# Performance work log

Measured on AMD Instinct MI355X. Metric: run time of the kernel, lower is better.

Reference implementation:

```python
import jax, jax.numpy as jnp
import numpy as np

# dims: batch, history P, horizon Q, hidden D, nodes N, cells C=H*W, Z channels
B_, P_, Q_, D_, N_, C_, H_, W_, CZ = 16, 12, 12, 64, 2000, 1024, 32, 32, 2
K_DIFF = 3  # max diffusion step of DCGRUCell -> K+1 Chebyshev terms


def _mlp2(x, w1, b1, w2, b2):
    return jax.nn.relu(x @ w1 + b1) @ w2 + b2


def _st_embedding(SE, TE, sw1, sb1, sw2, sb2, tw1, tb1, tw2, tb2):
    # GMAN-style spatio-temporal embedding: SE (M,D), TE (B,P,2) ints
    se = _mlp2(SE, sw1, sb1, sw2, sb2)                                  # (M, D)
    te = jnp.concatenate([jax.nn.one_hot(TE[..., 0], 7, dtype=SE.dtype),
                          jax.nn.one_hot(TE[..., 1], 288, dtype=SE.dtype)], axis=-1)
    te = _mlp2(te, tw1, tb1, tw2, tb2)                                  # (B, P, D)
    return se[None, None] + te[:, :, None, :]                           # (B, P, M, D)


def _scaled_laplacian(adj):
    # DCRNN 'laplacian' filter: L_tilde = 2 L / lambda_max - I, lambda_max ~= 2
    A = jnp.maximum(adj, adj.T)
    d = A.sum(axis=1)
    dinv = jnp.where(d > 0, jax.lax.rsqrt(d), 0.0)
    eye = jnp.eye(A.shape[0], dtype=A.dtype)
    L = eye - (dinv[:, None] * A) * dinv[None, :]
    return L - eye


def _gconv(x, L, K):
    # Chebyshev diffusion features: x (B,N,F) -> (B,N,F*(K+1))
    xs = [x, jnp.einsum('nm,bmf->bnf', L, x)]
    for _ in range(2, K + 1):
        xs.append(2.0 * jnp.einsum('nm,bmf->bnf', L, xs[-1]) - xs[-2])
    b, n, f = x.shape
    return jnp.stack(xs, axis=-1).reshape(b, n, f * (K + 1))


def _hard_sigmoid(x):
    return jnp.clip(0.2 * x + 0.5, 0.0, 1.0)


def _conv2d(x, w):
    return jax.lax.conv_general_dilated(x, w, (1, 1), 'SAME',
        dimension_numbers=('NHWC', 'HWIO', 'NHWC'))


def _forward(X, Z, TE, adj_gg, adj_gr, gumbel_noise, se_x, se_z, movement_logits,
             stex_se_w1, stex_se_b1, stex_se_w2, stex_se_b2,
             stex_te_w1, stex_te_b1, stex_te_w2, stex_te_b2,
             stez_se_w1, stez_se_b1, stez_se_w2, stez_se_b2,
             stez_te_w1, stez_te_b1, stez_te_w2, stez_te_b2,
             fcs_z_w1, fcs_z_b1, fcs_z_w2, fcs_z_b2,
             fcs_x_in_w1, fcs_x_in_b1, fcs_x_in_w2, fcs_x_in_b2,
             mov_fc_w, mov_fc_b,
             fcs_x_out_w1, fcs_x_out_b1, fcs_x_out_w2, fcs_x_out_b2,
             convlstm_wx, convlstm_wh,
             dcgru_gate_w, dcgru_gate_b, dcgru_cand_w, dcgru_cand_b):
    B = X.shape[0]
    TEp = TE.astype(jnp.int32)[:, :P_, :]
    # --- cell branch ---
    STEZ = _st_embedding(se_z, TEp, stez_se_w1, stez_se_b1, stez_se_w2, stez_se_b2,
                         stez_te_w1, stez_te_b1, stez_te_w2, stez_te_b2)
    Zf = _mlp2(Z, fcs_z_w1, fcs_z_b1, fcs_z_w2, fcs_z_b2) + STEZ          # (B,P,C,D)
    Zg = Zf.reshape(B, P_, H_, W_, D_)
    def clstm_step(carry, x):
        h, c = carry
        gates = _conv2d(x, convlstm_wx) + _conv2d(h, convlstm_wh)         # (B,H,W,4D)
        i, f, g, o = jnp.split(gates, 4, axis=-1)
        c = _hard_sigmoid(f) * c + _hard_sigmoid(i) * jnp.tanh(g)
        h = _hard_sigmoid(o) * jnp.tanh(c)
        return (h, c), h
    hc0 = (jnp.zeros((B, H_, W_, D_), X.dtype), jnp.zeros((B, H_, W_, D_), X.dtype))
    _, hs = jax.lax.scan(clstm_step, hc0, jnp.swapaxes(Zg, 0, 1))
    Zc = jnp.swapaxes(hs, 0, 1).reshape(B, P_, C_, D_)
    # gumbel-softmax routing over cells (soft, tau=1)
    g = -jnp.log(-jnp.log(gumbel_noise + 1e-20) + 1e-20)
    mZ = jax.nn.softmax(movement_logits + g, axis=-1)                     # (C,C)
    Zc = jnp.einsum('cd,bpdk->bpck', mZ, Zc)
    Zc = jax.nn.relu(Zc @ mov_fc_w + mov_fc_b)
    ZX = jnp.einsum('nc,bpck->bpnk', adj_gr, Zc)                          # (B,P,N,D)
    # --- node branch ---
    STEX = _st_embedding(se_x, TEp, stex_se_w1, stex_se_b1, stex_se_w2, stex_se_b2,
                         stex_te_w1, stex_te_b1, stex_te_w2, stex_te_b2)
    Xf = _mlp2(X[..., None], fcs_x_in_w1, fcs_x_in_b1, fcs_x_in_w2, fcs_x_in_b2) + STEX + ZX
    L = _scaled_laplacian(adj_gg)
    def dcgru_step(h, x):
        xh = jnp.concatenate([x, h], axis=-1)                             # (B,N,2D)
        ru = jax.nn.sigmoid(_gconv(xh, L, K_DIFF) @ dcgru_gate_w + dcgru_gate_b)
        r, u = jnp.split(ru, 2, axis=-1)
        cnd = jnp.tanh(_gconv(jnp.concatenate([x, r * h], axis=-1), L, K_DIFF)
                       @ dcgru_cand_w + dcgru_cand_b)
        return u * h + (1.0 - u) * cnd, None
    h_last, _ = jax.lax.scan(dcgru_step, jnp.zeros((B, N_, D_), X.dtype),
                             jnp.swapaxes(Xf, 0, 1))                      # (B,N,D)
    Y = _mlp2(h_last, fcs_x_out_w1, fcs_x_out_b1, fcs_x_out_w2, fcs_x_out_b2)  # (B,N,Q)
    return jnp.transpose(Y, (0, 2, 1))                                    # (B,Q,N)


def setup_inputs() -> dict:
    key = jax.random.key(0)
    ks = iter(jax.random.split(key, 64))
    def rn(shape, s=0.05):
        return jax.random.normal(next(ks), shape, dtype=jnp.float32) * s
    def ru(shape):
        return jax.random.uniform(next(ks), shape, dtype=jnp.float32)
    z = lambda *s: jnp.zeros(s, jnp.float32)
    NM = K_DIFF + 1
    inp = {
        'X': rn((B_, P_, N_), 1.0),
        'Z': rn((B_, P_, C_, CZ), 1.0),
        'TE': jax.random.randint(next(ks), (B_, P_ + Q_, 2), 0, 7, dtype=jnp.int32),
        'adj_gg': ru((N_, N_)),
        'adj_gr': ru((N_, C_)) * 0.01,
        'gumbel_noise': jnp.clip(ru((C_, C_)), 1e-6, 1.0 - 1e-6),
        'se_x': rn((N_, D_)), 'se_z': rn((C_, D_)),
        'movement_logits': rn((C_, C_)),
        'stex_se_w1': rn((D_, D_)), 'stex_se_b1': z(D_), 'stex_se_w2': rn((D_, D_)), 'stex_se_b2': z(D_),
        'stex_te_w1': rn((295, D_)), 'stex_te_b1': z(D_), 'stex_te_w2': rn((D_, D_)), 'stex_te_b2': z(D_),
        'stez_se_w1': rn((D_, D_)), 'stez_se_b1': z(D_), 'stez_se_w2': rn((D_, D_)), 'stez_se_b2': z(D_),
        'stez_te_w1': rn((295, D_)), 'stez_te_b1': z(D_), 'stez_te_w2': rn((D_, D_)), 'stez_te_b2': z(D_),
        'fcs_z_w1': rn((CZ, D_)), 'fcs_z_b1': z(D_), 'fcs_z_w2': rn((D_, D_)), 'fcs_z_b2': z(D_),
        'fcs_x_in_w1': rn((1, D_)), 'fcs_x_in_b1': z(D_), 'fcs_x_in_w2': rn((D_, D_)), 'fcs_x_in_b2': z(D_),
        'mov_fc_w': rn((D_, D_)), 'mov_fc_b': z(D_),
        'fcs_x_out_w1': rn((D_, D_)), 'fcs_x_out_b1': z(D_), 'fcs_x_out_w2': rn((D_, Q_)), 'fcs_x_out_b2': z(Q_),
        'convlstm_wx': rn((3, 3, D_, 4 * D_)), 'convlstm_wh': rn((3, 3, D_, 4 * D_)),
        'dcgru_gate_w': rn((2 * D_ * NM, 2 * D_)), 'dcgru_gate_b': z(2 * D_),
        'dcgru_cand_w': rn((2 * D_ * NM, D_)), 'dcgru_cand_b': z(D_),
    }
    return inp


def reference(X, Z, TE, adj_gg, adj_gr, gumbel_noise, se_x, se_z, movement_logits,
              stex_se_w1, stex_se_b1, stex_se_w2, stex_se_b2,
              stex_te_w1, stex_te_b1, stex_te_w2, stex_te_b2,
              stez_se_w1, stez_se_b1, stez_se_w2, stez_se_b2,
              stez_te_w1, stez_te_b1, stez_te_w2, stez_te_b2,
              fcs_z_w1, fcs_z_b1, fcs_z_w2, fcs_z_b2,
              fcs_x_in_w1, fcs_x_in_b1, fcs_x_in_w2, fcs_x_in_b2,
              mov_fc_w, mov_fc_b,
              fcs_x_out_w1, fcs_x_out_b1, fcs_x_out_w2, fcs_x_out_b2,
              convlstm_wx, convlstm_wh,
              dcgru_gate_w, dcgru_gate_b, dcgru_cand_w, dcgru_cand_b):
    return _forward(X, Z, TE, adj_gg, adj_gr, gumbel_noise, se_x, se_z, movement_logits,
                    stex_se_w1, stex_se_b1, stex_se_w2, stex_se_b2,
                    stex_te_w1, stex_te_b1, stex_te_w2, stex_te_b2,
                    stez_se_w1, stez_se_b1, stez_se_w2, stez_se_b2,
                    stez_te_w1, stez_te_b1, stez_te_w2, stez_te_b2,
                    fcs_z_w1, fcs_z_b1, fcs_z_w2, fcs_z_b2,
                    fcs_x_in_w1, fcs_x_in_b1, fcs_x_in_w2, fcs_x_in_b2,
                    mov_fc_w, mov_fc_b,
                    fcs_x_out_w1, fcs_x_out_b1, fcs_x_out_w2, fcs_x_out_b2,
                    convlstm_wx, convlstm_wh,
                    dcgru_gate_w, dcgru_gate_b, dcgru_cand_w, dcgru_cand_b)
```

## Files before the change

kernel.cpp:

```cpp
#include <hip/hip_runtime.h>
#include <hip/hip_bf16.h>
#include <math.h>

typedef _Float16 fp16;
typedef _Float16 f16x8 __attribute__((ext_vector_type(8)));
typedef float f32x4 __attribute__((ext_vector_type(4)));

#define BB 16
#define PP 12
#define QQ 12
#define NN 2000
#define CC 1024
#define GP 34
#define GP2 1156

static __device__ __forceinline__ float ldf(float v) { return v; }
static __device__ __forceinline__ float ldf(fp16 v) { return (float)v; }
static __device__ __forceinline__ void stf(float* p, float v) { *p = v; }
static __device__ __forceinline__ void stf(fp16* p, float v) { *p = (fp16)v; }

static __device__ __forceinline__ void gload_lds16(const fp16* g, fp16* l) {
  __builtin_amdgcn_global_load_lds(
      (const __attribute__((address_space(1))) void*)g,
      (__attribute__((address_space(3))) void*)l, 16, 0, 0);
}

__global__ void k_f2h(fp16* __restrict__ dst, const float* __restrict__ src, long long n) {
  long long i = (long long)blockIdx.x * 256 + threadIdx.x;
  if (i < n) dst[i] = (fp16)src[i];
}

__global__ void k_wcatT(fp16* __restrict__ dst, const float* __restrict__ w39,
                        const float* __restrict__ w40) {
  int i = blockIdx.x * 256 + threadIdx.x;
  if (i >= 1152 * 256) return;
  int n = i & 255, kk = i >> 8;
  float v = (kk < 576) ? w39[kk * 256 + n] : w40[(kk - 576) * 256 + n];
  dst[(long long)n * 1152 + kk] = (fp16)v;
}

__global__ void k_gru_repackT(fp16* __restrict__ dst, const float* __restrict__ src, int O) {
  int i = blockIdx.x * 256 + threadIdx.x;
  if (i >= O * 512) return;
  int d = i >> 9;
  int kc = i & 511;
  int t = kc >> 7;
  int c = kc & 127;
  dst[i] = (fp16)src[(c * 4 + t) * O + d];
}

__global__ void k_w2T(fp16* __restrict__ dst, const float* __restrict__ src) {
  int i = blockIdx.x * 256 + threadIdx.x;
  if (i >= 4096) return;
  int d = i >> 6, k = i & 63;
  dst[i] = (fp16)src[k * 64 + d];
}

__global__ void k_dinv(const float* __restrict__ adj, float* __restrict__ dinv) {
  int row = blockIdx.x;
  float s = 0.f;
  for (int j = threadIdx.x; j < NN; j += 256)
    s += fmaxf(adj[(long long)row * NN + j], adj[(long long)j * NN + row]);
  __shared__ float red[256];
  red[threadIdx.x] = s;
  __syncthreads();
  for (int st = 128; st > 0; st >>= 1) {
    if (threadIdx.x < st) red[threadIdx.x] += red[threadIdx.x + st];
    __syncthreads();
  }
  if (threadIdx.x == 0) {
    float d = red[0];
    dinv[row] = d > 0.f ? 1.0f / sqrtf(d) : 0.f;
  }
}

__global__ void k_L(const float* __restrict__ adj, const float* __restrict__ dinv,
                    fp16* __restrict__ Lh) {
  long long i = (long long)blockIdx.x * 256 + threadIdx.x;
  if (i >= (long long)NN * NN) return;
  int r = (int)(i / NN), c = (int)(i % NN);
  float a = fmaxf(adj[(long long)r * NN + c], adj[(long long)c * NN + r]);
  Lh[(long long)r * 2048 + c] = (fp16)(-dinv[r] * a * dinv[c]);
}

__global__ void k_subdiag(fp16* __restrict__ M2) {
  int i = blockIdx.x * 256 + threadIdx.x;
  if (i >= NN) return;
  M2[(long long)i * 2048 + i] = (fp16)((float)M2[(long long)i * 2048 + i] - 1.0f);
}

__global__ void k_gumbel_softmax(const float* __restrict__ ml, const float* __restrict__ gn,
                                 fp16* __restrict__ mZ) {
  int row = blockIdx.x;
  __shared__ float buf[CC];
  __shared__ float red[256];
  int t = threadIdx.x;
  float mx = -1e30f;
  for (int j = t; j < CC; j += 256) {
    float u = gn[(long long)row * CC + j];
    float g = -logf(-logf(u + 1e-20f) + 1e-20f);
    float v = ml[(long long)row * CC + j] + g;
    buf[j] = v;
    mx = fmaxf(mx, v);
  }
  red[t] = mx;
  __syncthreads();
  for (int st = 128; st > 0; st >>= 1) {
    if (t < st) red[t] = fmaxf(red[t], red[t + st]);
    __syncthreads();
  }
  mx = red[0];
  __syncthreads();
  float s = 0.f;
  for (int j = t; j < CC; j += 256) {
    float e = expf(buf[j] - mx);
    buf[j] = e;
    s += e;
  }
  red[t] = s;
  __syncthreads();
  for (int st = 128; st > 0; st >>= 1) {
    if (t < st) red[t] += red[t + st];
    __syncthreads();
  }
  float inv = 1.0f / red[0];
  for (int j = t; j < CC; j += 256) mZ[(long long)row * CC + j] = (fp16)(buf[j] * inv);
}

__global__ void k_te(const int* __restrict__ TE, const float* __restrict__ w1,
                     const float* __restrict__ b1, float* __restrict__ tmp) {
  int i = blockIdx.x * 256 + threadIdx.x;
  if (i >= BB * PP * 64) return;
  int j = i & 63;
  int bp = i >> 6;
  int b = bp / PP, p = bp % PP;
  int te0 = TE[(b * (PP + QQ) + p) * 2 + 0];
  int te1 = TE[(b * (PP + QQ) + p) * 2 + 1];
  float v = w1[te0 * 64 + j] + w1[(7 + te1) * 64 + j] + b1[j];
  tmp[i] = fmaxf(v, 0.f);
}

__global__ void k_addb(float* __restrict__ dst, const float* __restrict__ b, int n) {
  int i = blockIdx.x * 256 + threadIdx.x;
  if (i < n) dst[i] += b[i & 63];
}

__global__ void k_zf1(const float* __restrict__ Z, const float* __restrict__ w1,
                      const float* __restrict__ b1, fp16* __restrict__ tmp) {
  long long i = (long long)blockIdx.x * 256 + threadIdx.x;
  if (i >= (long long)BB * PP * CC * 64) return;
  int j = (int)(i & 63);
  long long row = i >> 6;
  float v = Z[row * 2 + 0] * w1[j] + Z[row * 2 + 1] * w1[64 + j] + b1[j];
  tmp[i] = (fp16)fmaxf(v, 0.f);
}

__global__ void k_add_stez(fp16* __restrict__ dst, const fp16* __restrict__ src,
                           const float* __restrict__ seZ, const float* __restrict__ teZ) {
  long long i = (long long)blockIdx.x * 256 + threadIdx.x;
  if (i >= (long long)BB * PP * CC * 64) return;
  int j = (int)(i & 63);
  long long row = i >> 6;
  int c = (int)(row & 1023);
  int bp = (int)(row >> 10);
  int pc = ((c >> 5) + 1) * GP + (c & 31) + 1;
  dst[((long long)bp * GP2 + pc) * 64 + j] =
      (fp16)((float)src[i] + seZ[c * 64 + j] + teZ[bp * 64 + j]);
}

template <typename TA, typename TB, typename TC>
__global__ __launch_bounds__(256) void gemm_t(
    const TA* __restrict__ A, int lda, long long sA,
    const TB* __restrict__ Bm, int ldb, long long sB,
    TC* Cm, int ldc, long long sC,
    const TC* S, long long sS,
    const float* __restrict__ bias,
    int M, int Ncols, int K, float alpha, float beta, int act) {
  int bz = blockIdx.z;
  A += (long long)bz * sA;
  Bm += (long long)bz * sB;
  Cm += (long long)bz * sC;
  if (S) S += (long long)bz * sS;
  const int row0 = blockIdx.x * 64, col0 = blockIdx.y * 64;
  __shared__ float As[16][68];
  __shared__ float Bs[16][68];
  int tid = threadIdx.x, tx = tid & 15, ty = tid >> 4;
  float acc[4][4] = {};
  for (int k0 = 0; k0 < K; k0 += 16) {
#pragma unroll
    for (int j = 0; j < 4; ++j) {
      int e = tid + 256 * j;
      int m = e >> 4, kk = e & 15;
      int gm = row0 + m;
      As[kk][m] = (gm < M) ? ldf(A[(long long)gm * lda + k0 + kk]) : 0.f;
    }
#pragma unroll
    for (int j = 0; j < 4; ++j) {
      int e = tid + 256 * j;
      int kk = e >> 6, n = e & 63;
      int gn = col0 + n;
      Bs[kk][n] = (gn < Ncols) ? ldf(Bm[(long long)(k0 + kk) * ldb + gn]) : 0.f;
    }
    __syncthreads();
#pragma unroll
    for (int kk = 0; kk < 16; ++kk) {
      float a[4], bb[4];
#pragma unroll
      for (int i = 0; i < 4; ++i) a[i] = As[kk][ty * 4 + i];
#pragma unroll
      for (int j = 0; j < 4; ++j) bb[j] = Bs[kk][tx * 4 + j];
#pragma unroll
      for (int i = 0; i < 4; ++i)
#pragma unroll
        for (int j = 0; j < 4; ++j) acc[i][j] = fmaf(a[i], bb[j], acc[i][j]);
    }
    __syncthreads();
  }
#pragma unroll
  for (int i = 0; i < 4; ++i) {
    int r = row0 + ty * 4 + i;
    if (r >= M) continue;
#pragma unroll
    for (int j = 0; j < 4; ++j) {
      int cn = col0 + tx * 4 + j;
      if (cn >= Ncols) continue;
      float v = alpha * acc[i][j];
      if (bias) v += bias[cn];
      if (S) v += beta * ldf(S[(long long)r * ldc + cn]);
      if (act == 1) v = fmaxf(v, 0.f);
      else if (act == 2) v = 1.f / (1.f + expf(-v));
      else if (act == 3) v = tanhf(v);
      stf(&Cm[(long long)r * ldc + cn], v);
    }
  }
}

template <int MT, int MODE>
__global__ __launch_bounds__(256) void mfma5(
    const fp16* __restrict__ A, int lda,
    const fp16* __restrict__ U0base, long long uZ, int bHi,
    const fp16* __restrict__ xB, long long xZ,
    const fp16* __restrict__ Tn, long long TnSlab,
    const fp16* __restrict__ Tn2, long long Tn2Slab,
    fp16* __restrict__ C, int ldc, long long cBatch,
    const float* __restrict__ bias,
    fp16* __restrict__ rhOut, const fp16* __restrict__ hIn,
    const fp16* __restrict__ uIn, long long uStride,
    int M, int Ncols, int K) {
  __shared__ fp16 As[MT][40];
  __shared__ fp16 Bs[64][40];
  const int z = blockIdx.z;
  const int gm0 = blockIdx.x * MT, n0 = blockIdx.y * 64;
  const fp16* U0z = U0base + (long long)z * uZ;
  const fp16* xBz = xB + (long long)z * xZ;
  C += (long long)z * cBatch;
  if (rhOut) rhOut += (long long)z * uZ;
  if (hIn) hIn += (long long)z * uZ;
  if (uIn) uIn += (long long)z * uStride;
  const int tid = threadIdx.x;
  const int lane = tid & 63, wv = tid >> 6;
  const int wr = wv >> 1, wc = wv & 1;
  const int quad = lane >> 4, ln = lane & 15;
  constexpr int WM = MT / 32;
  f32x4 acc[WM][2];
#pragma unroll
  for (int i = 0; i < WM; ++i)
#pragma unroll
    for (int j = 0; j < 2; ++j) acc[i][j] = (f32x4){0.f, 0.f, 0.f, 0.f};

  for (int k0 = 0; k0 < K; k0 += 32) {
#pragma unroll
    for (int i = 0; i < MT / 64; ++i) {
      int c = tid + 256 * i;
      int row = c >> 2, seg = c & 3;
      *(f16x8*)&As[row][seg * 8] =
          *(const f16x8*)(A + (long long)(gm0 + row) * lda + k0 + seg * 8);
    }
    {
      int slab = k0 >> 7;
      if (slab == 0) {
        int kin = k0 + (tid & 31);
        int ngrp = tid >> 5;
        int n = n0 + ngrp * 8;
        const fp16* src = (kin < 64) ? (xBz + (long long)kin * 2048 + n)
                                     : (U0z + (long long)(kin + bHi) * 2048 + n);
        f16x8 v = *(const f16x8*)src;
#pragma unroll
        for (int j = 0; j < 8; ++j) Bs[ngrp * 8 + j][tid & 31] = v[j];
      } else {
        int n = tid >> 2, seg = tid & 3;
        int kin0 = (k0 & 127) + seg * 8;
        long long node = n0 + n;
        const fp16* src;
        if (MODE == 1 || kin0 < 64)
          src = Tn + (long long)(slab - 1) * TnSlab + node * 2048 + z * 128 + kin0;
        else
          src = Tn2 + (long long)(slab - 1) * Tn2Slab + node * 1024 + z * 64 + (kin0 - 64);
        *(f16x8*)&Bs[n][seg * 8] = *(const f16x8*)src;
      }
    }
    __syncthreads();
    f16x8 af[WM], bf[2];
#pragma unroll
    for (int wm = 0; wm < WM; ++wm)
      af[wm] = *(const f16x8*)&As[wr * (MT / 2) + wm * 16 + ln][quad * 8];
#pragma unroll
    for (int wn = 0; wn < 2; ++wn)
      bf[wn] = *(const f16x8*)&Bs[wc * 32 + wn * 16 + ln][quad * 8];
#pragma unroll
    for (int wm = 0; wm < WM; ++wm)
#pragma unroll
      for (int wn = 0; wn < 2; ++wn)
        acc[wm][wn] =
            __builtin_amdgcn_mfma_f32_16x16x32_f16(af[wm], bf[wn], acc[wm][wn], 0, 0, 0);
    __syncthreads();
  }
#pragma unroll
  for (int wm = 0; wm < WM; ++wm) {
#pragma unroll
    for (int wn = 0; wn < 2; ++wn) {
#pragma unroll
      for (int r = 0; r < 4; ++r) {
        int gm = gm0 + wr * (MT / 2) + wm * 16 + quad * 4 + r;
        int gn = n0 + wc * 32 + wn * 16 + ln;
        if (gm < M && gn < Ncols) {
          float v = acc[wm][wn][r];
          v += bias[gm];
          if (MODE == 1) {
            v = 1.f / (1.f + expf(-v));
            C[(long long)gm * ldc + gn] = (fp16)v;
            if (gm < 64) {
              float h = (float)hIn[(long long)gm * 2048 + gn];
              rhOut[(long long)gm * 2048 + gn] = (fp16)(v * h);
            }
          } else {
            v = tanhf(v);
            float u = (float)uIn[(long long)(64 + gm) * NN + gn];
            long long ci = (long long)gm * ldc + gn;
            float h = (float)C[ci];
            C[ci] = (fp16)(u * h + (1.f - u) * v);
          }
        }
      }
    }
  }
}

template <int MT, int NT>
__global__ __launch_bounds__(256) void mfma3(
    const fp16* __restrict__ A, int lda, long long zA, int aMsh, long long aMslab,
    const fp16* __restrict__ B, int ldb, long long zB,
    fp16* __restrict__ C, int ldc, long long zC, int cMsh, long long cMslab, int cNsh,
    long long cNslab,
    const fp16* __restrict__ S, long long zS, float beta,
    const float* __restrict__ rowBias, long long zRB,
    const float* __restrict__ s2T, int s2ld,
    int M, int Ncols, int K, float alpha, int act) {
  __shared__ fp16 As[MT][40];
  __shared__ fp16 Bs[NT][40];
  const int z = blockIdx.z;
  const int gm0 = blockIdx.x * MT, n0 = blockIdx.y * NT;
  A += (long long)z * zA;
  B += (long long)z * zB;
  C += (long long)z * zC;
  if (S) S += (long long)z * zS;
  const int tid = threadIdx.x;
  const int lane = tid & 63, wv = tid >> 6;
  const int wr = wv >> 1, wc = wv & 1;
  const int quad = lane >> 4, ln = lane & 15;
  const unsigned aMmask = (1u << aMsh) - 1u;
  const unsigned cMmask = (1u << cMsh) - 1u;
  const unsigned cNmask = (1u << cNsh) - 1u;
  constexpr int WM = MT / 32, WN = NT / 32;
  f32x4 acc[WM][WN];
#pragma unroll
  for (int i = 0; i < WM; ++i)
#pragma unroll
    for (int j = 0; j < WN; ++j) acc[i][j] = (f32x4){0.f, 0.f, 0.f, 0.f};

  for (int k0 = 0; k0 < K; k0 += 32) {
#pragma unroll
    for (int i = 0; i < MT / 64; ++i) {
      int c = tid + 256 * i;
      int row = c >> 2, seg = c & 3;
      int gm = gm0 + row;
      int kk0 = k0 + seg * 8;
      const fp16* src = A + ((long long)((unsigned)gm >> aMsh)) * aMslab +
                        (long long)(gm & aMmask) * lda + kk0;
      if (gm < M && kk0 + 8 <= K) {
        *(f16x8*)&As[row][seg * 8] = *(const f16x8*)src;
      } else {
#pragma unroll
        for (int j = 0; j < 8; ++j)
          As[row][seg * 8 + j] = (gm < M && kk0 + j < K) ? src[j] : (fp16)0.f;
      }
    }
#pragma unroll
    for (int i = 0; i < NT / 64; ++i) {
      int c = tid + 256 * i;
      int n = c >> 2, seg = c & 3;
      int gn = n0 + n;
      int kk0 = k0 + seg * 8;
      const fp16* src = B + (long long)gn * ldb + kk0;
      if (gn < Ncols && kk0 + 8 <= K) {
        *(f16x8*)&Bs[n][seg * 8] = *(const f16x8*)src;
      } else {
#pragma unroll
        for (int j = 0; j < 8; ++j)
          Bs[n][seg * 8 + j] = (gn < Ncols && kk0 + j < K) ? src[j] : (fp16)0.f;
      }
    }
    __syncthreads();
    f16x8 af[WM], bf[WN];
#pragma unroll
    for (int wm = 0; wm < WM; ++wm)
      af[wm] = *(const f16x8*)&As[wr * (MT / 2) + wm * 16 + ln][quad * 8];
#pragma unroll
    for (int wn = 0; wn < WN; ++wn)
      bf[wn] = *(const f16x8*)&Bs[wc * (NT / 2) + wn * 16 + ln][quad * 8];
#pragma unroll
    for (int wm = 0; wm < WM; ++wm)
#pragma unroll
      for (int wn = 0; wn < WN; ++wn)
        acc[wm][wn] =
            __builtin_amdgcn_mfma_f32_16x16x32_f16(af[wm], bf[wn], acc[wm][wn], 0, 0, 0);
    __syncthreads();
  }
#pragma unroll
  for (int wm = 0; wm < WM; ++wm) {
#pragma unroll
    for (int wn = 0; wn < WN; ++wn) {
#pragma unroll
      for (int r = 0; r < 4; ++r) {
        int gm = gm0 + wr * (MT / 2) + wm * 16 + quad * 4 + r;
        int gn = n0 + wc * (NT / 2) + wn * 16 + ln;
        if (gm < M && gn < Ncols) {
          float v = alpha * acc[wm][wn][r];
          if (rowBias) v += rowBias[(long long)z * zRB + gm];
          if (s2T) v += s2T[(long long)gn * s2ld + gm];
          long long ci = ((long long)((unsigned)gm >> cMsh)) * cMslab +
                         (long long)(gm & cMmask) * ldc +
                         ((long long)((unsigned)gn >> cNsh)) * cNslab + (gn & cNmask);
          if (S) v += beta * (float)S[ci];
          if (act == 1) v = fmaxf(v, 0.f);
          else if (act == 2) v = 1.f / (1.f + expf(-v));
          else if (act == 3) v = tanhf(v);
          C[ci] = (fp16)v;
        }
      }
    }
  }
}

template <int MT, int NT>
__global__ __launch_bounds__(256) void mfma4(
    const fp16* __restrict__ base0, const fp16* __restrict__ base1, int rsh, int ssh,
    long long z0, long long z1, int lda,
    const fp16* __restrict__ B, int ldb, long long zB,
    fp16* __restrict__ C, int ldc, long long zC, int cMsh, long long cMslab, int cNsh,
    long long cNslab,
    const fp16* __restrict__ S, float alpha, float beta, int K) {
  __shared__ fp16 As[2][MT * 32];
  __shared__ fp16 Bs[2][NT * 32];
  const int tid = threadIdx.x;
  const int z = blockIdx.z;
  const int gm0 = blockIdx.x * MT, n0 = blockIdx.y * NT;
  B += (long long)z * zB;
  C += (long long)z * zC;
  if (S) S += (long long)z * zC;
  const unsigned cMmask = (1u << cMsh) - 1u;
  const unsigned cNmask = (1u << cNsh) - 1u;
  const int lane = tid & 63, wv = tid >> 6;
  const int wr = wv >> 1, wc = wv & 1;
  const int quad = lane >> 4, ln = lane & 15;
  constexpr int WM = MT / 32, WN = NT / 32;

  const fp16* aSrc[MT / 64];
  const fp16* bSrc[NT / 64];
#pragma unroll
  for (int i = 0; i < MT / 64; ++i) {
    int c = i * 256 + tid;
    int row = c >> 2;
    int lseg = (c & 3) ^ (row & 3);
    int gm = gm0 + row;
    unsigned b = (unsigned)gm >> rsh;
    unsigned wi = (unsigned)gm & ((1u << rsh) - 1u);
    unsigned sel = wi >> ssh;
    unsigned r = wi & ((1u << ssh) - 1u);
    const fp16* ab = sel ? (base1 + (long long)b * z1) : (base0 + (long long)b * z0);
    aSrc[i] = ab + (long long)r * lda + lseg * 8;
  }
#pragma unroll
  for (int i = 0; i < NT / 64; ++i) {
    int c = i * 256 + tid;
    int row = c >> 2;
    int lseg = (c & 3) ^ (row & 3);
    bSrc[i] = B + (long long)(n0 + row) * ldb + lseg * 8;
  }

  f32x4 acc[WM][WN];
#pragma unroll
  for (int i = 0; i < WM; ++i)
#pragma unroll
    for (int j = 0; j < WN; ++j) acc[i][j] = (f32x4){0.f, 0.f, 0.f, 0.f};

  const int sw = (quad ^ (ln & 3)) << 3;

#pragma unroll
  for (int i = 0; i < MT / 64; ++i) gload_lds16(aSrc[i], &As[0][(i * 256 + tid) * 8]);
#pragma unroll
  for (int i = 0; i < NT / 64; ++i) gload_lds16(bSrc[i], &Bs[0][(i * 256 + tid) * 8]);

  const int nk = K >> 5;
  for (int t = 0; t < nk; ++t) {
    const int buf = t & 1;
    __syncthreads();
    if (t + 1 < nk) {
      const int k1 = (t + 1) * 32;
#pragma unroll
      for (int i = 0; i < MT / 64; ++i)
        gload_lds16(aSrc[i] + k1, &As[buf ^ 1][(i * 256 + tid) * 8]);
#pragma unroll
      for (int i = 0; i < NT / 64; ++i)
        gload_lds16(bSrc[i] + k1, &Bs[buf ^ 1][(i * 256 + tid) * 8]);
    }
    f16x8 af[WM], bf[WN];
#pragma unroll
    for (int wm = 0; wm < WM; ++wm) {
      int row = wr * (MT / 2) + wm * 16 + ln;
      af[wm] = *(const f16x8*)&As[buf][row * 32 + sw];
    }
#pragma unroll
    for (int wn = 0; wn < WN; ++wn) {
      int row = wc * (NT / 2) + wn * 16 + ln;
      bf[wn] = *(const f16x8*)&Bs[buf][row * 32 + sw];
    }
#pragma unroll
    for (int wm = 0; wm < WM; ++wm)
#pragma unroll
      for (int wn = 0; wn < WN; ++wn)
        acc[wm][wn] =
            __builtin_amdgcn_mfma_f32_16x16x32_f16(af[wm], bf[wn], acc[wm][wn], 0, 0, 0);
  }
#pragma unroll
  for (int wm = 0; wm < WM; ++wm)
#pragma unroll
    for (int wn = 0; wn < WN; ++wn)
#pragma unroll
      for (int r = 0; r < 4; ++r) {
        int gm = gm0 + wr * (MT / 2) + wm * 16 + quad * 4 + r;
        int gn = n0 + wc * (NT / 2) + wn * 16 + ln;
        long long ci = ((long long)((unsigned)gm >> cMsh)) * cMslab +
                       (long long)(gm & cMmask) * ldc +
                       ((long long)((unsigned)gn >> cNsh)) * cNslab + (gn & cNmask);
        float v = alpha * acc[wm][wn][r];
        if (S) v += beta * (float)S[ci];
        C[ci] = (fp16)v;
      }
}

template <int MT, int NT>
__global__ __launch_bounds__(256) void mfma6(
    const fp16* __restrict__ A, int lda,
    const fp16* __restrict__ b0, const fp16* __restrict__ b1, int rsh, int ssh,
    long long z0, long long z1, int ldb,
    fp16* __restrict__ C, int ldc, int cMsh, long long cMslab,
    int K) {
  __shared__ fp16 As[2][MT * 32];
  __shared__ fp16 Bs[2][NT * 32];
  const int tid = threadIdx.x;
  const int gm0 = blockIdx.x * MT, n0 = blockIdx.y * NT;
  const unsigned cMmask = (1u << cMsh) - 1u;
  const int lane = tid & 63, wv = tid >> 6;
  const int wr = wv >> 1, wc = wv & 1;
  const int quad = lane >> 4, ln = lane & 15;
  constexpr int WM = MT / 32, WN = NT / 32;

  const fp16* aSrc[MT / 64];
  const fp16* bSrc[NT / 64];
#pragma unroll
  for (int i = 0; i < MT / 64; ++i) {
    int c = i * 256 + tid;
    int row = c >> 2;
    int lseg = (c & 3) ^ (row & 3);
    aSrc[i] = A + (long long)(gm0 + row) * lda + lseg * 8;
  }
#pragma unroll
  for (int i = 0; i < NT / 64; ++i) {
    int c = i * 256 + tid;
    int row = c >> 2;
    int lseg = (c & 3) ^ (row & 3);
    int gn = n0 + row;
    unsigned b = (unsigned)gn >> rsh;
    unsigned wi = (unsigned)gn & ((1u << rsh) - 1u);
    unsigned sel = wi >> ssh;
    unsigned r = wi & ((1u << ssh) - 1u);
    const fp16* bb = sel ? (b1 + (long long)b * z1) : (b0 + (long long)b * z0);
    bSrc[i] = bb + (long long)r * ldb + lseg * 8;
  }

  f32x4 acc[WM][WN];
#pragma unroll
  for (int i = 0; i < WM; ++i)
#pragma unroll
    for (int j = 0; j < WN; ++j) acc[i][j] = (f32x4){0.f, 0.f, 0.f, 0.f};

  const int sw = (quad ^ (ln & 3)) << 3;

#pragma unroll
  for (int i = 0; i < MT / 64; ++i) gload_lds16(aSrc[i], &As[0][(i * 256 + tid) * 8]);
#pragma unroll
  for (int i = 0; i < NT / 64; ++i) gload_lds16(bSrc[i], &Bs[0][(i * 256 + tid) * 8]);

  const int nk = K >> 5;
  for (int t = 0; t < nk; ++t) {
    const int buf = t & 1;
    __syncthreads();
    if (t + 1 < nk) {
      const int k1 = (t + 1) * 32;
#pragma unroll
      for (int i = 0; i < MT / 64; ++i)
        gload_lds16(aSrc[i] + k1, &As[buf ^ 1][(i * 256 + tid) * 8]);
#pragma unroll
      for (int i = 0; i < NT / 64; ++i)
        gload_lds16(bSrc[i] + k1, &Bs[buf ^ 1][(i * 256 + tid) * 8]);
    }
    f16x8 af[WM], bf[WN];
#pragma unroll
    for (int wm = 0; wm < WM; ++wm) {
      int row = wr * (MT / 2) + wm * 16 + ln;
      af[wm] = *(const f16x8*)&As[buf][row * 32 + sw];
    }
#pragma unroll
    for (int wn = 0; wn < WN; ++wn) {
      int row = wc * (NT / 2) + wn * 16 + ln;
      bf[wn] = *(const f16x8*)&Bs[buf][row * 32 + sw];
    }
#pragma unroll
    for (int wm = 0; wm < WM; ++wm)
#pragma unroll
      for (int wn = 0; wn < WN; ++wn)
        acc[wm][wn] =
            __builtin_amdgcn_mfma_f32_16x16x32_f16(af[wm], bf[wn], acc[wm][wn], 0, 0, 0);
  }
#pragma unroll
  for (int wm = 0; wm < WM; ++wm)
#pragma unroll
    for (int wn = 0; wn < WN; ++wn)
#pragma unroll
      for (int r = 0; r < 4; ++r) {
        int gm = gm0 + wr * (MT / 2) + wm * 16 + quad * 4 + r;
        int gn = n0 + wc * (NT / 2) + wn * 16 + ln;
        long long ci = ((long long)((unsigned)gm >> cMsh)) * cMslab +
                       (long long)(gm & cMmask) * ldc + gn;
        C[ci] = (fp16)acc[wm][wn][r];
      }
}

__global__ __launch_bounds__(256) void k_zxtfin(
    const fp16* __restrict__ w2T, const fp16* __restrict__ Tmat,
    fp16* __restrict__ ZXt, const float* __restrict__ teXb, const float* __restrict__ seX) {
  __shared__ fp16 As[64][72];
  __shared__ fp16 Bs[128][72];
  const int z = blockIdx.z;
  const int n0 = blockIdx.y * 128;
  const fp16* Tz = Tmat + (long long)z * 2048 * 64;
  fp16* Cz = ZXt + (long long)z * 64 * 2048;
  const float* tb = teXb + z * 64;
  const int tid = threadIdx.x;
  const int lane = tid & 63, wv = tid >> 6;
  const int wr = wv >> 1, wc = wv & 1;
  const int quad = lane >> 4, ln = lane & 15;
#pragma unroll
  for (int i = 0; i < 2; ++i) {
    int c = tid + 256 * i;
    int row = c >> 3, seg = c & 7;
    *(f16x8*)&As[row][seg * 8] = *(const f16x8*)(w2T + row * 64 + seg * 8);
  }
#pragma unroll
  for (int i = 0; i < 4; ++i) {
    int c = tid + 256 * i;
    int row = c >> 3, seg = c & 7;
    *(f16x8*)&Bs[row][seg * 8] =
        *(const f16x8*)(Tz + (long long)(n0 + row) * 64 + seg * 8);
  }
  __syncthreads();
  f32x4 acc[2][4];
#pragma unroll
  for (int i = 0; i < 2; ++i)
#pragma unroll
    for (int j = 0; j < 4; ++j) acc[i][j] = (f32x4){0.f, 0.f, 0.f, 0.f};
#pragma unroll
  for (int kt = 0; kt < 2; ++kt) {
    f16x8 af[2], bf[4];
#pragma unroll
    for (int wm = 0; wm < 2; ++wm)
      af[wm] = *(const f16x8*)&As[wr * 32 + wm * 16 + ln][kt * 32 + quad * 8];
#pragma unroll
    for (int wn = 0; wn < 4; ++wn)
      bf[wn] = *(const f16x8*)&Bs[wc * 64 + wn * 16 + ln][kt * 32 + quad * 8];
#pragma unroll
    for (int wm = 0; wm < 2; ++wm)
#pragma unroll
      for (int wn = 0; wn < 4; ++wn)
        acc[wm][wn] =
            __builtin_amdgcn_mfma_f32_16x16x32_f16(af[wm], bf[wn], acc[wm][wn], 0, 0, 0);
  }
#pragma unroll
  for (int wm = 0; wm < 2; ++wm)
#pragma unroll
    for (int wn = 0; wn < 4; ++wn)
#pragma unroll
      for (int r = 0; r < 4; ++r) {
        int gm = wr * 32 + wm * 16 + quad * 4 + r;
        int gn = n0 + wc * 64 + wn * 16 + ln;
        long long ci = (long long)gm * 2048 + gn;
        float v = 0.f;
        if (gn < NN)
          v = acc[wm][wn][r] + (float)Cz[ci] + tb[gm] + seX[(long long)gn * 64 + gm];
        Cz[ci] = (fp16)v;
      }
}

__global__ __launch_bounds__(256) void k_conv4(
    const fp16* __restrict__ Zfp, const fp16* __restrict__ hp,
    const fp16* __restrict__ wcatT, fp16* __restrict__ gates, int p) {
  __shared__ fp16 As[2][128 * 32];
  __shared__ fp16 Bs[2][64 * 32];
  const int gm0 = blockIdx.x * 128, n0 = blockIdx.y * 64;
  const int tid = threadIdx.x;
  const int lane = tid & 63, wv = tid >> 6;
  const int wr = wv >> 1, wc = wv & 1;
  const int quad = lane >> 4, ln = lane & 15;

  long long aZ[2], aH[2];
#pragma unroll
  for (int i = 0; i < 2; ++i) {
    int c = tid + 256 * i;
    int row = c >> 2;
    int lseg = (c & 3) ^ (row & 3);
    int m = gm0 + row;
    int b = m >> 10, y = (m >> 5) & 31, x = m & 31;
    int pc = (y + 1) * GP + (x + 1);
    aZ[i] = ((long long)(b * PP + p) * GP2 + pc) * 64 + lseg * 8;
    aH[i] = ((long long)b * GP2 + pc) * 64 + lseg * 8;
  }
  const fp16* bBase;
  {
    int row = tid >> 2;
    int lseg = (tid & 3) ^ (row & 3);
    bBase = wcatT + (long long)(n0 + row) * 1152 + lseg * 8;
  }
  f32x4 acc[4][2];
#pragma unroll
  for (int i = 0; i < 4; ++i)
#pragma unroll
    for (int j = 0; j < 2; ++j) acc[i][j] = (f32x4){0.f, 0.f, 0.f, 0.f};

  auto stage = [&](int t, int buf) {
    int tap = (t >> 1) % 9, half = t & 1;
    int srcsel = t >= 18;
    int off = ((tap / 3 - 1) * GP + (tap % 3 - 1)) * 64 + half * 32;
#pragma unroll
    for (int i = 0; i < 2; ++i) {
      const fp16* src = srcsel ? (hp + aH[i] + off) : (Zfp + aZ[i] + off);
      gload_lds16(src, &As[buf][(i * 256 + tid) * 8]);
    }
    gload_lds16(bBase + t * 32, &Bs[buf][tid * 8]);
  };
  stage(0, 0);
  const int sw = (quad ^ (ln & 3)) << 3;
  for (int t = 0; t < 36; ++t) {
    const int buf = t & 1;
    __syncthreads();
    if (t + 1 < 36) stage(t + 1, buf ^ 1);
    f16x8 af[4], bf[2];
#pragma unroll
    for (int wm = 0; wm < 4; ++wm) {
      int row = wr * 64 + wm * 16 + ln;
      af[wm] = *(const f16x8*)&As[buf][row * 32 + sw];
    }
#pragma unroll
    for (int wn = 0; wn < 2; ++wn) {
      int row = wc * 32 + wn * 16 + ln;
      bf[wn] = *(const f16x8*)&Bs[buf][row * 32 + sw];
    }
#pragma unroll
    for (int wm = 0; wm < 4; ++wm)
#pragma unroll
      for (int wn = 0; wn < 2; ++wn)
        acc[wm][wn] =
            __builtin_amdgcn_mfma_f32_16x16x32_f16(af[wm], bf[wn], acc[wm][wn], 0, 0, 0);
  }
#pragma unroll
  for (int wm = 0; wm < 4; ++wm)
#pragma unroll
    for (int wn = 0; wn < 2; ++wn)
#pragma unroll
      for (int r = 0; r < 4; ++r) {
        int gm = gm0 + wr * 64 + wm * 16 + quad * 4 + r;
        int gn = n0 + wc * 32 + wn * 16 + ln;
        gates[(long long)gm * 256 + gn] = (fp16)acc[wm][wn][r];
      }
}

__global__ void k_clstm_update(const fp16* __restrict__ gates, float* __restrict__ c,
                               fp16* __restrict__ h, fp16* __restrict__ ZclT, int p) {
  long long i = (long long)blockIdx.x * 256 + threadIdx.x;
  if (i >= (long long)BB * CC * 64) return;
  int d = (int)(i & 63);
  long long bc = i >> 6;
  int b = (int)(bc >> 10);
  int cell = (int)(bc & 1023);
  const fp16* g = gates + (((long long)b * CC) + cell) * 256;
  float gi = (float)g[d], gf = (float)g[64 + d], gg = (float)g[128 + d],
        go = (float)g[192 + d];
  float hs_f = fminf(fmaxf(0.2f * gf + 0.5f, 0.f), 1.f);
  float hs_i = fminf(fmaxf(0.2f * gi + 0.5f, 0.f), 1.f);
  float hs_o = fminf(fmaxf(0.2f * go + 0.5f, 0.f), 1.f);
  float cv = hs_f * c[i] + hs_i * tanhf(gg);
  c[i] = cv;
  float hv = hs_o * tanhf(cv);
  int pc = ((cell >> 5) + 1) * GP + (cell & 31) + 1;
  h[((long long)b * GP2 + pc) * 64 + d] = (fp16)hv;
  ZclT[(((long long)(b * PP + p)) * 64 + d) * CC + cell] = (fp16)hv;
}

__global__ void k_tmat(const float* __restrict__ X, const float* __restrict__ w1,
                       const float* __restrict__ b1, fp16* __restrict__ T, long long nrows) {
  long long i = (long long)blockIdx.x * 256 + threadIdx.x;
  if (i >= nrows * 64) return;
  int j = (int)(i & 63);
  long long row = i >> 6;
  int z = (int)(row / NN);
  int n = (int)(row - (long long)z * NN);
  T[(((long long)z * 2048) + n) * 64 + j] = (fp16)fmaxf(X[row] * w1[j] + b1[j], 0.f);
}

__global__ void k_trT(const fp16* __restrict__ U0, float* __restrict__ htmp) {
  long long i = (long long)blockIdx.x * 256 + threadIdx.x;
  if (i >= (long long)BB * NN * 64) return;
  int d = (int)(i & 63);
  long long bn = i >> 6;
  int b = (int)(bn / NN);
  int n = (int)(bn % NN);
  htmp[i] = (float)U0[((long long)b * 192 + 64 + d) * 2048 + n];
}

__global__ void k_out(const float* __restrict__ Y, float* __restrict__ out) {
  int i = blockIdx.x * 256 + threadIdx.x;
  if (i >= BB * QQ * NN) return;
  int n = i % NN;
  int bq = i / NN;
  int b = bq / QQ, q = bq % QQ;
  out[i] = Y[((long long)b * NN + n) * 12 + q];
}

template <typename TA, typename TB, typename TC>
static void launch_gemm(hipStream_t stream, const TA* A, int lda, long long sA,
                        const TB* Bm, int ldb, long long sB, TC* Cm, int ldc, long long sC,
                        const TC* S, long long sS, const float* bias, int M, int Nc, int K,
                        float alpha, float beta, int act, int batch) {
  dim3 g((M + 63) / 64, (Nc + 63) / 64, batch);
  gemm_t<TA, TB, TC><<<g, dim3(256), 0, stream>>>(A, lda, sA, Bm, ldb, sB, Cm, ldc, sC, S,
                                                  sS, bias, M, Nc, K, alpha, beta, act);
}

extern "C" void kernel_launch(void* const* d_in, const int* in_sizes, int n_in,
                              void* d_out, int out_size, void* d_ws, size_t ws_size,
                              hipStream_t stream) {
  char* base = (char*)d_ws;
  size_t off = 0;
  auto alloc_bytes = [&](size_t nb) -> char* {
    char* p = base + off;
    off += (nb + 255) & ~(size_t)255;
    return p;
  };
  auto allocf = [&](size_t n) -> float* { return (float*)alloc_bytes(n * 4); };
  auto alloch = [&](size_t n) -> fp16* { return (fp16*)alloc_bytes(n * 2); };

  const float* X = (const float*)d_in[0];
  const float* Z = (const float*)d_in[1];
  const int* TE = (const int*)d_in[2];
  const float* adj_gg = (const float*)d_in[3];
  const float* adj_gr = (const float*)d_in[4];
  const float* gumbel = (const float*)d_in[5];
  const float* se_x = (const float*)d_in[6];
  const float* se_z = (const float*)d_in[7];
  const float* movement = (const float*)d_in[8];
  auto W = [&](int i) { return (const float*)d_in[i]; };

  fp16* wcatT = alloch((size_t)256 * 1152);
  fp16* gwT = alloch(128 * 512);
  fp16* cwT = alloch(64 * 512);
  fp16* w2T = alloch(64 * 64);
  fp16* w2mT = alloch(64 * 64);
  float* dinv = allocf(NN);
  fp16* LMall = alloch((size_t)6144 * 2048);
  fp16* mZh = alloch((size_t)CC * CC);
  fp16* agh2 = alloch((size_t)2048 * CC);
  float* seZ = allocf(CC * 64);
  float* teZ = allocf(BB * PP * 64);
  float* seX = allocf(NN * 64);
  float* teXb = allocf(BB * PP * 64);
  float* mtmp = allocf(NN * 64);
  float* tetmp = allocf(BB * PP * 64);
  fp16* ruT = alloch((size_t)BB * 128 * NN);
  char* pool = alloc_bytes(50331648);
  fp16* Uall = (fp16*)pool;
  fp16* gates = (fp16*)pool;
  fp16* chh = (fp16*)(pool + 8388608);
  float* ccc = (float*)(pool + 12582912);
  fp16* Zmix = (fp16*)pool;
  fp16* ZmovT = (fp16*)(pool + 25165824);
  fp16* zpool = alloch((size_t)BB * PP * 64 * 2048);
  fp16* Zfp = zpool;
  fp16* ZXt = zpool;
  fp16* Zc = alloch((size_t)BB * PP * CC * 64);

  if (off > ws_size) return;

  const long long uB = 192LL * 2048;
  const long long USL = 16LL * uB;
  const long long ZXB = 12LL * 64 * 2048;
  fp16* Lh = LMall;
  fp16* M2h = LMall + 2048LL * 2048;
  fp16* M3h = LMall + 4096LL * 2048;
  const int KCH = 2016;

  k_wcatT<<<dim3(1152), dim3(256), 0, stream>>>(wcatT, W(39), W(40));
  k_gru_repackT<<<dim3(256), dim3(256), 0, stream>>>(gwT, W(41), 128);
  k_gru_repackT<<<dim3(128), dim3(256), 0, stream>>>(cwT, W(43), 64);
  k_w2T<<<dim3(16), dim3(256), 0, stream>>>(w2T, W(31));
  k_w2T<<<dim3(16), dim3(256), 0, stream>>>(w2mT, W(33));
  k_dinv<<<dim3(NN), dim3(256), 0, stream>>>(adj_gg, dinv);
  hipMemsetAsync(LMall, 0, (size_t)6144 * 2048 * 2, stream);
  k_L<<<dim3((NN * NN + 255) / 256), dim3(256), 0, stream>>>(adj_gg, dinv, Lh);
  mfma4<64, 128><<<dim3(32, 16, 1), dim3(256), 0, stream>>>(
      Lh, Lh, 31, 31, 0LL, 0LL, 2048, Lh, 2048, 0LL, M2h, 2048, 0LL, 31, 0LL, 31, 0LL,
      (const fp16*)nullptr, 2.f, 0.f, KCH);
  k_subdiag<<<dim3((NN + 255) / 256), dim3(256), 0, stream>>>(M2h);
  mfma4<64, 128><<<dim3(32, 16, 1), dim3(256), 0, stream>>>(
      Lh, Lh, 31, 31, 0LL, 0LL, 2048, M2h, 2048, 0LL, M3h, 2048, 0LL, 31, 0LL, 31, 0LL,
      (const fp16*)Lh, 2.f, -1.f, KCH);
  k_gumbel_softmax<<<dim3(CC), dim3(256), 0, stream>>>(movement, gumbel, mZh);
  k_f2h<<<dim3((NN * CC + 255) / 256), dim3(256), 0, stream>>>(agh2, adj_gr,
                                                               (long long)NN * CC);
  hipMemsetAsync(agh2 + (size_t)NN * CC, 0, (size_t)(2048 - NN) * CC * 2, stream);

  launch_gemm(stream, se_z, 64, 0LL, W(17), 64, 0LL, mtmp, 64, 0LL, (float*)nullptr, 0LL,
              W(18), CC, 64, 64, 1.f, 0.f, 1, 1);
  launch_gemm(stream, (const float*)mtmp, 64, 0LL, W(19), 64, 0LL, seZ, 64, 0LL,
              (float*)nullptr, 0LL, W(20), CC, 64, 64, 1.f, 0.f, 0, 1);
  k_te<<<dim3((BB * PP * 64 + 255) / 256), dim3(256), 0, stream>>>(TE, W(21), W(22), tetmp);
  launch_gemm(stream, (const float*)tetmp, 64, 0LL, W(23), 64, 0LL, teZ, 64, 0LL,
              (float*)nullptr, 0LL, W(24), BB * PP, 64, 64, 1.f, 0.f, 0, 1);
  launch_gemm(stream, se_x, 64, 0LL, W(9), 64, 0LL, mtmp, 64, 0LL, (float*)nullptr, 0LL,
              W(10), NN, 64, 64, 1.f, 0.f, 1, 1);
  launch_gemm(stream, (const float*)mtmp, 64, 0LL, W(11), 64, 0LL, seX, 64, 0LL,
              (float*)nullptr, 0LL, W(12), NN, 64, 64, 1.f, 0.f, 0, 1);
  k_te<<<dim3((BB * PP * 64 + 255) / 256), dim3(256), 0, stream>>>(TE, W(13), W(14), tetmp);
  launch_gemm(stream, (const float*)tetmp, 64, 0LL, W(15), 64, 0LL, teXb, 64, 0LL,
              (float*)nullptr, 0LL, W(16), BB * PP, 64, 64, 1.f, 0.f, 0, 1);
  k_addb<<<dim3((BB * PP * 64 + 255) / 256), dim3(256), 0, stream>>>(teXb, W(32),
                                                                     BB * PP * 64);

  long long nZ = (long long)BB * PP * CC * 64;
  k_zf1<<<dim3((int)((nZ + 255) / 256)), dim3(256), 0, stream>>>(Z, W(25), W(26), Zc);
  launch_gemm(stream, (const fp16*)Zc, 64, 0LL, W(27), 64, 0LL, (fp16*)pool, 64, 0LL,
              (fp16*)nullptr, 0LL, W(28), BB * PP * CC, 64, 64, 1.f, 0.f, 0, 1);
  hipMemsetAsync(zpool, 0, (size_t)BB * PP * GP2 * 64 * 2, stream);
  k_add_stez<<<dim3((int)((nZ + 255) / 256)), dim3(256), 0, stream>>>(Zfp, (fp16*)pool,
                                                                      seZ, teZ);

  hipMemsetAsync(chh, 0, (size_t)BB * GP2 * 64 * 2, stream);
  hipMemsetAsync(ccc, 0, (size_t)BB * CC * 64 * 4, stream);
  for (int p = 0; p < PP; ++p) {
    k_conv4<<<dim3(BB * CC / 128, 4), dim3(256), 0, stream>>>(Zfp, chh, wcatT, gates, p);
    k_clstm_update<<<dim3((int)(((long long)BB * CC * 64 + 255) / 256)), dim3(256), 0,
                     stream>>>(gates, ccc, chh, Zc, p);
  }

  mfma4<128, 64><<<dim3(8, 1, 192), dim3(256), 0, stream>>>(
      mZh, mZh, 31, 31, 0LL, 0LL, CC, (const fp16*)Zc, CC, (long long)64 * CC, Zmix, 64,
      (long long)CC * 64, 31, 0LL, 31, 0LL, (const fp16*)nullptr, 1.f, 0.f, CC);
  mfma3<64, 128><<<dim3(1, 8, 192), dim3(256), 0, stream>>>(
      w2mT, 64, 0LL, 31, 0LL, Zmix, 64, (long long)CC * 64, ZmovT, CC, (long long)64 * CC,
      31, 0LL, 31, 0LL, (const fp16*)nullptr, 0LL, 0.f, W(34), 0LL, nullptr, 0, 64, CC, 64,
      1.f, 1);

  mfma4<128, 128><<<dim3(96, 16, 1), dim3(256), 0, stream>>>(
      ZmovT, ZmovT, 31, 31, 0LL, 0LL, 1024, agh2, 1024, 0LL, ZXt, 2048, 0LL, 31, 0LL, 31,
      0LL, (const fp16*)nullptr, 1.f, 0.f, 1024);

  fp16* Tmat = Zc;
  for (int half = 0; half < 2; ++half) {
    long long z0 = 96LL * half;
    k_tmat<<<dim3((int)((96LL * NN * 64 + 255) / 256)), dim3(256), 0, stream>>>(
        X + z0 * NN, W(29), W(30), Tmat, 96LL * NN);
    k_zxtfin<<<dim3(1, 16, 96), dim3(256), 0, stream>>>(
        w2T, Tmat, ZXt + z0 * 64 * 2048, teXb + z0 * 64, seX);
  }

  fp16* U0 = Uall;
  fp16* Tn = Uall + USL;
  fp16* Tn2 = Uall + 3 * USL;
  const long long TnSlab = 2048LL * 2048;
  const long long Tn2Slab = 2048LL * 1024;
  hipMemsetAsync(U0, 0, (size_t)USL * 2, stream);
  for (int p = 0; p < PP; ++p) {
    const fp16* xP = ZXt + (long long)p * 64 * 2048;
    mfma6<128, 128><<<dim3(48, 16), dim3(256), 0, stream>>>(
        LMall, 2048, xP, U0 + 64 * 2048, 7, 6, ZXB, uB, 2048, Tn, 2048, 11, TnSlab, KCH);
    mfma5<128, 1><<<dim3(1, 32, BB), dim3(256), 0, stream>>>(
        gwT, 512, U0, uB, 0, xP, ZXB, Tn, TnSlab, (const fp16*)nullptr, 0LL, ruT, NN,
        (long long)128 * NN, W(42), U0 + 128 * 2048, U0 + 64 * 2048,
        (const fp16*)nullptr, 0LL, 128, NN, 512);
    mfma6<128, 128><<<dim3(48, 8), dim3(256), 0, stream>>>(
        LMall, 2048, U0 + 128 * 2048, U0 + 128 * 2048, 6, 6, uB, uB, 2048, Tn2, 1024, 11,
        Tn2Slab, KCH);
    mfma5<64, 2><<<dim3(1, 32, BB), dim3(256), 0, stream>>>(
        cwT, 512, U0, uB, 64, xP, ZXB, Tn, TnSlab, Tn2, Tn2Slab, U0 + 64 * 2048, 2048, uB,
        W(44), (fp16*)nullptr, (const fp16*)nullptr, (const fp16*)ruT, (long long)128 * NN,
        64, NN, 512);
  }

  float* htmp = (float*)Zc;
  float* out1 = (float*)(Zc + 5120000);
  float* out2 = (float*)(Zc + 10240000);
  k_trT<<<dim3((int)(((long long)BB * NN * 64 + 255) / 256)), dim3(256), 0, stream>>>(U0,
                                                                                      htmp);
  launch_gemm(stream, (const float*)htmp, 64, 0LL, W(35), 64, 0LL, out1, 64, 0LL,
              (float*)nullptr, 0LL, W(36), BB * NN, 64, 64, 1.f, 0.f, 1, 1);
  launch_gemm(stream, (const float*)out1, 64, 0LL, W(37), 12, 0LL, out2, 12, 0LL,
              (float*)nullptr, 0LL, W(38), BB * NN, 12, 64, 1.f, 0.f, 0, 1);
  k_out<<<dim3((BB * QQ * NN + 255) / 256), dim3(256), 0, stream>>>(out2, (float*)d_out);
}
```

Baseline: 3.118 ms.

## Hoist input diffusion out of GRU loop and double-buffer gate GEMM

Precomputes the Chebyshev diffusion of the input features for all 12 timesteps in one large batched GEMM before the recurrent loop, so each step only diffuses the hidden state (half the columns). The gate/candidate GEMM kernel is rewritten with double-buffered LDS staging via direct global-to-LDS loads and an XOR swizzle to reduce bank conflicts, dropping one barrier per k-step. A fallback path keeps the old per-step diffusion when workspace is too small. It costs extra workspace for the hoisted slab and uses a strided layout for reading it.

Result: faster. 2.998 ms (-3.9%).

```diff
diff --git a/kernel.cpp b/kernel.cpp
--- a/kernel.cpp
+++ b/kernel.cpp
@@ -236,21 +236,21 @@
 }
 
 template <int MT, int MODE>
-__global__ __launch_bounds__(256) void mfma5(
-    const fp16* __restrict__ A, int lda,
+__global__ __launch_bounds__(256) void mfma7(
+    const fp16* __restrict__ A,
     const fp16* __restrict__ U0base, long long uZ, int bHi,
     const fp16* __restrict__ xB, long long xZ,
-    const fp16* __restrict__ Tn, long long TnSlab,
-    const fp16* __restrict__ Tn2, long long Tn2Slab,
+    const fp16* __restrict__ Xc, long long XcSlab, int Xcld, int Xczmul,
+    const fp16* __restrict__ Hc, long long HcSlab, int Hcld, int Hczmul,
     fp16* __restrict__ C, int ldc, long long cBatch,
     const float* __restrict__ bias,
     fp16* __restrict__ rhOut, const fp16* __restrict__ hIn,
     const fp16* __restrict__ uIn, long long uStride,
-    int M, int Ncols, int K) {
-  __shared__ fp16 As[MT][40];
-  __shared__ fp16 Bs[64][40];
+    int M, int Ncols) {
+  __shared__ fp16 As[2][MT * 32];
+  __shared__ fp16 Bs[2][64 * 32];
   const int z = blockIdx.z;
-  const int gm0 = blockIdx.x * MT, n0 = blockIdx.y * 64;
+  const int n0 = blockIdx.y * 64;
   const fp16* U0z = U0base + (long long)z * uZ;
   const fp16* xBz = xB + (long long)z * xZ;
   C += (long long)z * cBatch;
@@ -262,58 +262,80 @@
   const int wr = wv >> 1, wc = wv & 1;
   const int quad = lane >> 4, ln = lane & 15;
   constexpr int WM = MT / 32;
+
+  const fp16* aSrc[MT / 64];
+#pragma unroll
+  for (int i = 0; i < MT / 64; ++i) {
+    int c = i * 256 + tid;
+    int row = c >> 2;
+    int lseg = (c & 3) ^ (row & 3);
+    aSrc[i] = A + (long long)row * 512 + lseg * 8;
+  }
+  const int brow = tid >> 2;
+  const int blseg = (tid & 3) ^ (brow & 3);
+  const long long bnode = n0 + brow;
+
   f32x4 acc[WM][2];
 #pragma unroll
   for (int i = 0; i < WM; ++i)
 #pragma unroll
     for (int j = 0; j < 2; ++j) acc[i][j] = (f32x4){0.f, 0.f, 0.f, 0.f};
 
-  for (int k0 = 0; k0 < K; k0 += 32) {
-#pragma unroll
-    for (int i = 0; i < MT / 64; ++i) {
-      int c = tid + 256 * i;
-      int row = c >> 2, seg = c & 3;
-      *(f16x8*)&As[row][seg * 8] =
-          *(const f16x8*)(A + (long long)(gm0 + row) * lda + k0 + seg * 8);
-    }
-    {
+  auto stage = [&](int t, int buf) {
+    const int k0 = t * 32;
+#pragma unroll
+    for (int i = 0; i < MT / 64; ++i)
+      gload_lds16(aSrc[i] + k0, &As[buf][(i * 256 + tid) * 8]);
+    if (k0 < 128) {
+      int kin = k0 + (tid & 31);
+      int ngrp = tid >> 5;
+      int n = n0 + ngrp * 8;
+      const fp16* src = (kin < 64) ? (xBz + (long long)kin * 2048 + n)
+                                   : (U0z + (long long)(kin + bHi) * 2048 + n);
+      f16x8 v = *(const f16x8*)src;
+      int kk = tid & 31;
+#pragma unroll
+      for (int j = 0; j < 8; ++j) {
+        int rn = ngrp * 8 + j;
+        Bs[buf][rn * 32 + ((((kk >> 3) ^ (rn & 3)) << 3) | (kk & 7))] = v[j];
+      }
+    } else {
       int slab = k0 >> 7;
-      if (slab == 0) {
-        int kin = k0 + (tid & 31);
-        int ngrp = tid >> 5;
-        int n = n0 + ngrp * 8;
-        const fp16* src = (kin < 64) ? (xBz + (long long)kin * 2048 + n)
-                                     : (U0z + (long long)(kin + bHi) * 2048 + n);
-        f16x8 v = *(const f16x8*)src;
-#pragma unroll
-        for (int j = 0; j < 8; ++j) Bs[ngrp * 8 + j][tid & 31] = v[j];
-      } else {
-        int n = tid >> 2, seg = tid & 3;
-        int kin0 = (k0 & 127) + seg * 8;
-        long long node = n0 + n;
-        const fp16* src;
-        if (MODE == 1 || kin0 < 64)
-          src = Tn + (long long)(slab - 1) * TnSlab + node * 2048 + z * 128 + kin0;
-        else
-          src = Tn2 + (long long)(slab - 1) * Tn2Slab + node * 1024 + z * 64 + (kin0 - 64);
-        *(f16x8*)&Bs[n][seg * 8] = *(const f16x8*)src;
-      }
-    }
+      int kin = (k0 & 127) + blseg * 8;
+      const fp16* src;
+      if (kin < 64)
+        src = Xc + (long long)(slab - 1) * XcSlab + bnode * Xcld +
+              (long long)z * Xczmul + kin;
+      else
+        src = Hc + (long long)(slab - 1) * HcSlab + bnode * Hcld +
+              (long long)z * Hczmul + (kin - 64);
+      gload_lds16(src, &Bs[buf][tid * 8]);
+    }
+  };
+
+  const int sw = (quad ^ (ln & 3)) << 3;
+  stage(0, 0);
+  for (int t = 0; t < 16; ++t) {
+    const int buf = t & 1;
     __syncthreads();
+    if (t + 1 < 16) stage(t + 1, buf ^ 1);
     f16x8 af[WM], bf[2];
 #pragma unroll
-    for (int wm = 0; wm < WM; ++wm)
-      af[wm] = *(const f16x8*)&As[wr * (MT / 2) + wm * 16 + ln][quad * 8];
-#pragma unroll
-    for (int wn = 0; wn < 2; ++wn)
-      bf[wn] = *(const f16x8*)&Bs[wc * 32 + wn * 16 + ln][quad * 8];
+    for (int wm = 0; wm < WM; ++wm) {
+      int row = wr * (MT / 2) + wm * 16 + ln;
+      af[wm] = *(const f16x8*)&As[buf][row * 32 + sw];
+    }
+#pragma unroll
+    for (int wn = 0; wn < 2; ++wn) {
+      int row = wc * 32 + wn * 16 + ln;
+      bf[wn] = *(const f16x8*)&Bs[buf][row * 32 + sw];
+    }
 #pragma unroll
     for (int wm = 0; wm < WM; ++wm)
 #pragma unroll
       for (int wn = 0; wn < 2; ++wn)
         acc[wm][wn] =
             __builtin_amdgcn_mfma_f32_16x16x32_f16(af[wm], bf[wn], acc[wm][wn], 0, 0, 0);
-    __syncthreads();
   }
 #pragma unroll
   for (int wm = 0; wm < WM; ++wm) {
@@ -321,7 +343,7 @@
     for (int wn = 0; wn < 2; ++wn) {
 #pragma unroll
       for (int r = 0; r < 4; ++r) {
-        int gm = gm0 + wr * (MT / 2) + wm * 16 + quad * 4 + r;
+        int gm = wr * (MT / 2) + wm * 16 + quad * 4 + r;
         int gn = n0 + wc * 32 + wn * 16 + ln;
         if (gm < M && gn < Ncols) {
           float v = acc[wm][wn][r];
@@ -920,6 +942,11 @@
 
   if (off > ws_size) return;
 
+  const long long TnXSlab = 2048LL * 12288;
+  size_t tnxBytes = ((size_t)3 * TnXSlab * 2 + 255) & ~(size_t)255;
+  fp16* TnX = (fp16*)(base + off);
+  const bool hoist = (off + tnxBytes) <= ws_size;
+
   const long long uB = 192LL * 2048;
   const long long USL = 16LL * uB;
   const long long ZXB = 12LL * 64 * 2048;
@@ -1006,23 +1033,55 @@
   fp16* Tn = Uall + USL;
   fp16* Tn2 = Uall + 3 * USL;
   const long long TnSlab = 2048LL * 2048;
+  const long long TnHSlab = 2048LL * 1024;
   const long long Tn2Slab = 2048LL * 1024;
   hipMemsetAsync(U0, 0, (size_t)USL * 2, stream);
+
+  if (hoist) {
+    mfma6<128, 128><<<dim3(48, 96), dim3(256), 0, stream>>>(
+        LMall, 2048, ZXt, ZXt, 31, 31, 0LL, 0LL, 2048, TnX, 12288, 11, TnXSlab, KCH);
+  }
+
   for (int p = 0; p < PP; ++p) {
     const fp16* xP = ZXt + (long long)p * 64 * 2048;
-    mfma6<128, 128><<<dim3(48, 16), dim3(256), 0, stream>>>(
-        LMall, 2048, xP, U0 + 64 * 2048, 7, 6, ZXB, uB, 2048, Tn, 2048, 11, TnSlab, KCH);
-    mfma5<128, 1><<<dim3(1, 32, BB), dim3(256), 0, stream>>>(
-        gwT, 512, U0, uB, 0, xP, ZXB, Tn, TnSlab, (const fp16*)nullptr, 0LL, ruT, NN,
-        (long long)128 * NN, W(42), U0 + 128 * 2048, U0 + 64 * 2048,
-        (const fp16*)nullptr, 0LL, 128, NN, 512);
+    if (hoist) {
+      mfma6<128, 128><<<dim3(48, 8), dim3(256), 0, stream>>>(
+          LMall, 2048, U0 + 64 * 2048, U0 + 64 * 2048, 6, 6, uB, uB, 2048, Tn, 1024, 11,
+          TnHSlab, KCH);
+      mfma7<128, 1><<<dim3(1, 32, BB), dim3(256), 0, stream>>>(
+          gwT, U0, uB, 0, xP, ZXB,
+          TnX + (long long)p * 64, TnXSlab, 12288, 768,
+          Tn, TnHSlab, 1024, 64,
+          ruT, NN, (long long)128 * NN, W(42), U0 + 128 * 2048, U0 + 64 * 2048,
+          (const fp16*)nullptr, 0LL, 128, NN);
+    } else {
+      mfma6<128, 128><<<dim3(48, 16), dim3(256), 0, stream>>>(
+          LMall, 2048, xP, U0 + 64 * 2048, 7, 6, ZXB, uB, 2048, Tn, 2048, 11, TnSlab, KCH);
+      mfma7<128, 1><<<dim3(1, 32, BB), dim3(256), 0, stream>>>(
+          gwT, U0, uB, 0, xP, ZXB,
+          Tn, TnSlab, 2048, 128,
+          Tn + 64, TnSlab, 2048, 128,
+          ruT, NN, (long long)128 * NN, W(42), U0 + 128 * 2048, U0 + 64 * 2048,
+          (const fp16*)nullptr, 0LL, 128, NN);
+    }
     mfma6<128, 128><<<dim3(48, 8), dim3(256), 0, stream>>>(
         LMall, 2048, U0 + 128 * 2048, U0 + 128 * 2048, 6, 6, uB, uB, 2048, Tn2, 1024, 11,
         Tn2Slab, KCH);
-    mfma5<64, 2><<<dim3(1, 32, BB), dim3(256), 0, stream>>>(
-        cwT, 512, U0, uB, 64, xP, ZXB, Tn, TnSlab, Tn2, Tn2Slab, U0 + 64 * 2048, 2048, uB,
-        W(44), (fp16*)nullptr, (const fp16*)nullptr, (const fp16*)ruT, (long long)128 * NN,
-        64, NN, 512);
+    if (hoist) {
+      mfma7<64, 2><<<dim3(1, 32, BB), dim3(256), 0, stream>>>(
+          cwT, U0, uB, 64, xP, ZXB,
+          TnX + (long long)p * 64, TnXSlab, 12288, 768,
+          Tn2, Tn2Slab, 1024, 64,
+          U0 + 64 * 2048, 2048, uB, W(44), (fp16*)nullptr, (const fp16*)nullptr,
+          (const fp16*)ruT, (long long)128 * NN, 64, NN);
+    } else {
+      mfma7<64, 2><<<dim3(1, 32, BB), dim3(256), 0, stream>>>(
+          cwT, U0, uB, 64, xP, ZXB,
+          Tn, TnSlab, 2048, 128,
+          Tn2, Tn2Slab, 1024, 64,
+          U0 + 64 * 2048, 2048, uB, W(44), (fp16*)nullptr, (const fp16*)nullptr,
+          (const fp16*)ruT, (long long)128 * NN, 64, NN);
+    }
   }
 
   float* htmp = (float*)Zc;
```
